# Kernel tuning notes

Measured on AMD Instinct MI355X. Metric: run time of the kernel, lower is better.

The kernel has to match this reference:

```python
import jax, jax.numpy as jnp
import numpy as np

N, E = 50000, 800000
D, DE = 128, 64
BN_EPS = 1e-5


def _bn(h, gamma, beta):
    # BatchNorm1d in training mode: biased batch statistics over the node axis
    mu = jnp.mean(h, axis=0)
    var = jnp.var(h, axis=0)
    return (h - mu) * jax.lax.rsqrt(var + BN_EPS) * gamma + beta


def setup_inputs() -> dict:
    key = jax.random.key(0)
    ks = jax.random.split(key, 12)
    s = lambda d: 1.0 / np.sqrt(d)
    return {
        "x": jax.random.normal(ks[0], (N, D), jnp.float32),
        "edge_index": jax.random.randint(ks[1], (2, E), 0, N, jnp.int64),
        "edge_attr_processed": jax.random.normal(ks[2], (E, DE), jnp.float32),
        # GINEConv edge linear: edge_dim -> node_dim
        "We": jax.random.uniform(ks[3], (D, DE), jnp.float32, -s(DE), s(DE)),
        "be": jnp.zeros((D,), jnp.float32),
        # MLP: Linear(D, 2D) -> BN(2D) -> ReLU -> Linear(2D, D)
        "W1": jax.random.uniform(ks[4], (2 * D, D), jnp.float32, -s(D), s(D)),
        "b1": jnp.zeros((2 * D,), jnp.float32),
        "g1": jnp.ones((2 * D,), jnp.float32),
        "beta1": jnp.zeros((2 * D,), jnp.float32),
        "W2": jax.random.uniform(ks[5], (D, 2 * D), jnp.float32, -s(2 * D), s(2 * D)),
        "b2": jnp.zeros((D,), jnp.float32),
        # outer BatchNorm(D)
        "g2": jnp.ones((D,), jnp.float32),
        "beta2": jnp.zeros((D,), jnp.float32),
        # GINE trainable eps (init 0.0)
        "eps": jnp.zeros((), jnp.float32),
    }


def reference(x, edge_index, edge_attr_processed, We, be, W1, b1, g1, beta1,
              W2, b2, g2, beta2, eps):
    src, dst = edge_index[0], edge_index[1]
    # GINEConv message: ReLU(x_j + Lin(edge_attr)); gather + edge add + relu
    msg = jax.nn.relu(x[src] + edge_attr_processed @ We.T + be)  # [E, D]
    # scatter-add aggregation at destination nodes
    agg = jax.ops.segment_sum(msg, dst, num_segments=x.shape[0])  # [N, D]
    h = (1.0 + eps) * x + agg
    # MLP: Linear -> BN -> ReLU -> Linear
    h = jax.nn.relu(_bn(h @ W1.T + b1, g1, beta1)) @ W2.T + b2
    # outer BN -> ReLU (dropout is identity at inference)
    return jax.nn.relu(_bn(h, g2, beta2))
```

## Files before the change

kernel.cpp:

```cpp
#include <hip/hip_runtime.h>
#include <stdint.h>
#include <stddef.h>


#define NN 50000
#define EE 800000
#define DD 128
#define DE 64
#define H1 256
#define NGRP 3125

typedef __attribute__((ext_vector_type(8))) short short8;
typedef __attribute__((ext_vector_type(4))) float floatx4;

__device__ __forceinline__ short f2bf(float f) {
    union { float f; uint32_t u; } v; v.f = f;
    return (short)((v.u + 0x7FFFu + ((v.u >> 16) & 1u)) >> 16);
}
__device__ __forceinline__ float bf2f(uint16_t u) {
    union { uint32_t u; float f; } v; v.u = (uint32_t)u << 16;
    return v.f;
}

__global__ __launch_bounds__(256) void swz_all_kernel(
    const float* __restrict__ We, const float* __restrict__ W1,
    const float* __restrict__ W2, short* __restrict__ dst) {
    int idx = blockIdx.x * 256 + threadIdx.x;
    if (idx >= 73728) return;
    const float* src; int KC, K, local; short* dp; bool efeat = false;
    if (idx < 8192)       { src = We; KC = 2; K = 64;  local = idx;          dp = dst; efeat = true; }
    else if (idx < 40960) { src = W1; KC = 4; K = 128; local = idx - 8192;  dp = dst + 8192; }
    else                  { src = W2; KC = 8; K = 256; local = idx - 40960; dp = dst + 40960; }
    int j = local & 7;
    int lane = (local >> 3) & 63;
    int f = local >> 9;
    int kc = f % KC;
    int nt = f / KC;
    int n = efeat ? ((lane & 15) * 8 + nt) : (nt * 16 + (lane & 15));
    int k = kc * 32 + ((lane >> 4) & 3) * 8 + j;
    dp[local] = f2bf(src[(size_t)n * K + k]);
}

__global__ __launch_bounds__(256) void count_kernel(const int* __restrict__ ei,
                                                    uint32_t* __restrict__ deg) {
    int e = blockIdx.x * 256 + threadIdx.x;
    atomicAdd(&deg[ei[EE + e]], 1u);
}

__global__ __launch_bounds__(256) void scan1_kernel(const uint32_t* __restrict__ deg,
                                                    uint32_t* __restrict__ partial) {
    __shared__ uint32_t ls[256];
    int i = blockIdx.x * 256 + threadIdx.x;
    ls[threadIdx.x] = deg[i];
    __syncthreads();
    for (int s = 128; s > 0; s >>= 1) {
        if (threadIdx.x < s) ls[threadIdx.x] += ls[threadIdx.x + s];
        __syncthreads();
    }
    if (threadIdx.x == 0) partial[blockIdx.x] = ls[0];
}

__global__ __launch_bounds__(256) void scan2_kernel(uint32_t* __restrict__ partial) {
    __shared__ uint32_t ls[196];
    if (threadIdx.x < 196) ls[threadIdx.x] = partial[threadIdx.x];
    __syncthreads();
    if (threadIdx.x == 0) {
        uint32_t run = 0;
        for (int i = 0; i < 196; ++i) { uint32_t t = ls[i]; ls[i] = run; run += t; }
    }
    __syncthreads();
    if (threadIdx.x < 196) partial[threadIdx.x] = ls[threadIdx.x];
}

__global__ __launch_bounds__(256) void scan3_kernel(const uint32_t* __restrict__ deg,
                                                    const uint32_t* __restrict__ partial,
                                                    uint32_t* __restrict__ base,
                                                    uint32_t* __restrict__ cursor) {
    __shared__ uint32_t ls[256];
    int i = blockIdx.x * 256 + threadIdx.x;
    uint32_t v = (i < NN) ? deg[i] : 0u;
    ls[threadIdx.x] = v;
    __syncthreads();
    for (int off = 1; off < 256; off <<= 1) {
        uint32_t t = (threadIdx.x >= off) ? ls[threadIdx.x - off] : 0u;
        __syncthreads();
        ls[threadIdx.x] += t;
        __syncthreads();
    }
    if (i < NN) {
        uint32_t b = partial[blockIdx.x] + ls[threadIdx.x] - v;
        base[i] = b;
        cursor[i] = b;
    } else if (i == NN) {
        base[NN] = EE;
    }
}

__global__ __launch_bounds__(256) void pos_kernel(const int* __restrict__ ei,
                                                  uint32_t* __restrict__ cursor,
                                                  uint32_t* __restrict__ pos) {
    int e = blockIdx.x * 256 + threadIdx.x;
    pos[e] = atomicAdd(&cursor[ei[EE + e]], 1u);
}

#define EDGE_GPW 5
__global__ __launch_bounds__(256) void edge_kernel(
    const float* __restrict__ x,
    const int* __restrict__ ei,
    const float* __restrict__ ea,
    const short* __restrict__ weswz,
    const float* __restrict__ be,
    const uint32_t* __restrict__ pos,
    uint16_t* __restrict__ msg)
{
    const int wave = threadIdx.x >> 6;
    const int lane = threadIdx.x & 63;
    const int l16 = lane & 15;
    const int q = lane >> 4;

    const short8* wp = (const short8*)weswz;
    short8 bfr[16];
#pragma unroll
    for (int f = 0; f < 16; ++f) bfr[f] = wp[f * 64 + lane];
    floatx4 bv0 = *(const floatx4*)(be + l16 * 8);
    floatx4 bv1 = *(const floatx4*)(be + l16 * 8 + 4);

    const int gbase = (blockIdx.x * 4 + wave) * EDGE_GPW;
    int sidx[4];
#pragma unroll
    for (int r = 0; r < 4; ++r) sidx[r] = ei[gbase * 16 + q * 4 + r];

#pragma unroll
    for (int g = 0; g < EDGE_GPW; ++g) {
        const int e0 = (gbase + g) * 16;
        floatx4 xa[4], xb[4];
#pragma unroll
        for (int r = 0; r < 4; ++r) {
            const float* xr = x + (size_t)sidx[r] * DD + l16 * 8;
            xa[r] = *(const floatx4*)(xr);
            xb[r] = *(const floatx4*)(xr + 4);
        }
        int sidxn[4];
        if (g + 1 < EDGE_GPW) {
#pragma unroll
            for (int r = 0; r < 4; ++r) sidxn[r] = ei[e0 + 16 + q * 4 + r];
        }
        uint32_t ppv[4];
#pragma unroll
        for (int r = 0; r < 4; ++r) ppv[r] = pos[e0 + q * 4 + r];

        const float* earow = ea + (size_t)(e0 + l16) * DE + q * 8;
        floatx4 p0 = *(const floatx4*)(earow);
        floatx4 p1 = *(const floatx4*)(earow + 4);
        floatx4 p2 = *(const floatx4*)(earow + 32);
        floatx4 p3 = *(const floatx4*)(earow + 36);
        short8 af0, af1;
#pragma unroll
        for (int j = 0; j < 4; ++j) {
            af0[j]     = f2bf(p0[j]);
            af0[j + 4] = f2bf(p1[j]);
            af1[j]     = f2bf(p2[j]);
            af1[j + 4] = f2bf(p3[j]);
        }
        floatx4 acc[8];
#pragma unroll
        for (int t = 0; t < 8; ++t) {
            floatx4 z = {0.f, 0.f, 0.f, 0.f};
            z = __builtin_amdgcn_mfma_f32_16x16x32_bf16(af0, bfr[t * 2], z, 0, 0, 0);
            acc[t] = __builtin_amdgcn_mfma_f32_16x16x32_bf16(af1, bfr[t * 2 + 1], z, 0, 0, 0);
        }
#pragma unroll
        for (int r = 0; r < 4; ++r) {
            uint32_t pk[4];
#pragma unroll
            for (int tt = 0; tt < 4; ++tt) {
                float X0 = (tt < 2) ? xa[r][2 * tt]     : xb[r][2 * tt - 4];
                float X1 = (tt < 2) ? xa[r][2 * tt + 1] : xb[r][2 * tt - 3];
                float B0 = (tt < 2) ? bv0[2 * tt]       : bv1[2 * tt - 4];
                float B1 = (tt < 2) ? bv0[2 * tt + 1]   : bv1[2 * tt - 3];
                float v0 = fmaxf(acc[2 * tt][r]     + B0 + X0, 0.f);
                float v1 = fmaxf(acc[2 * tt + 1][r] + B1 + X1, 0.f);
                pk[tt] = (uint32_t)(uint16_t)f2bf(v0) | ((uint32_t)(uint16_t)f2bf(v1) << 16);
            }
            uint4 val = {pk[0], pk[1], pk[2], pk[3]};
            *(uint4*)(msg + (size_t)ppv[r] * DD + l16 * 8) = val;
        }
        if (g + 1 < EDGE_GPW) {
#pragma unroll
            for (int r = 0; r < 4; ++r) sidx[r] = sidxn[r];
        }
    }
}

#define ACC8(u) do { \
    s0 += bf2f((uint16_t)((u).x & 0xFFFFu)); s1 += bf2f((uint16_t)((u).x >> 16)); \
    s2 += bf2f((uint16_t)((u).y & 0xFFFFu)); s3 += bf2f((uint16_t)((u).y >> 16)); \
    s4 += bf2f((uint16_t)((u).z & 0xFFFFu)); s5 += bf2f((uint16_t)((u).z >> 16)); \
    s6 += bf2f((uint16_t)((u).w & 0xFFFFu)); s7 += bf2f((uint16_t)((u).w >> 16)); } while (0)

__global__ __launch_bounds__(256) void reduce_kernel(
    const uint16_t* __restrict__ msg,
    const uint32_t* __restrict__ basep,
    const float* __restrict__ x,
    const float* __restrict__ epsp,
    uint16_t* __restrict__ hbf)
{
    const int n = blockIdx.x * 4 + (threadIdx.x >> 6);
    const int lane = threadIdx.x & 63;
    const int l16 = lane & 15;
    const int q = lane >> 4;
    const uint32_t b0 = basep[n];
    const uint32_t d = basep[n + 1] - b0;
    const uint4* bp = (const uint4*)((const uint32_t*)msg + (size_t)b0 * 64) + lane;
    float s0 = 0.f, s1 = 0.f, s2 = 0.f, s3 = 0.f;
    float s4 = 0.f, s5 = 0.f, s6 = 0.f, s7 = 0.f;
    const uint32_t nb = d >> 2;
    const uint32_t rem = d & 3u;
    uint32_t i = 0;
    for (; i + 2 <= nb; i += 2) {
        uint4 a = bp[(size_t)i * 64];
        uint4 b = bp[(size_t)(i + 1) * 64];
        ACC8(a); ACC8(b);
    }
    if (i < nb) { uint4 a = bp[(size_t)i * 64]; ACC8(a); }
    if ((uint32_t)q < rem) { uint4 a = bp[(size_t)nb * 64]; ACC8(a); }
    s0 += __shfl_xor(s0, 16); s0 += __shfl_xor(s0, 32);
    s1 += __shfl_xor(s1, 16); s1 += __shfl_xor(s1, 32);
    s2 += __shfl_xor(s2, 16); s2 += __shfl_xor(s2, 32);
    s3 += __shfl_xor(s3, 16); s3 += __shfl_xor(s3, 32);
    s4 += __shfl_xor(s4, 16); s4 += __shfl_xor(s4, 32);
    s5 += __shfl_xor(s5, 16); s5 += __shfl_xor(s5, 32);
    s6 += __shfl_xor(s6, 16); s6 += __shfl_xor(s6, 32);
    s7 += __shfl_xor(s7, 16); s7 += __shfl_xor(s7, 32);
    const float c1 = 1.0f + epsp[0];
    const float2 xv = *(const float2*)(x + (size_t)n * DD + (l16 * 4 + q) * 2);
    float a0 = (q == 0) ? s0 : (q == 1) ? s2 : (q == 2) ? s4 : s6;
    float a1 = (q == 0) ? s1 : (q == 1) ? s3 : (q == 2) ? s5 : s7;
    uint32_t pk = (uint32_t)(uint16_t)f2bf(c1 * xv.x + a0) |
                  ((uint32_t)(uint16_t)f2bf(c1 * xv.y + a1) << 16);
    ((uint32_t*)hbf)[(size_t)n * 64 + l16 * 4 + q] = pk;
}

__global__ __launch_bounds__(256) void gemm1_kernel(
    const uint16_t* __restrict__ hbf,
    const short* __restrict__ w1swz,
    const float* __restrict__ b1,
    uint16_t* __restrict__ t1,
    float* __restrict__ gsum,
    float* __restrict__ gsq)
{
    __shared__ float ls[H1];
    __shared__ float ls2[H1];
    const int tid = threadIdx.x;
    ls[tid] = 0.f; ls2[tid] = 0.f;
    __syncthreads();

    const int wave = tid >> 6;
    const int lane = tid & 63;
    const int l16 = lane & 15;
    const int q = lane >> 4;
    const short8* wp = (const short8*)w1swz;

    const int grp = blockIdx.x * 4 + wave;
    if (grp < NGRP) {
        const int n0 = grp * 16;
        const uint16_t* hr = hbf + (size_t)(n0 + l16) * DD + q * 8;
        short8 af[4];
#pragma unroll
        for (int kc = 0; kc < 4; ++kc) af[kc] = *(const short8*)(hr + kc * 32);
#pragma unroll
        for (int nt = 0; nt < 16; ++nt) {
            floatx4 acc = {0.f, 0.f, 0.f, 0.f};
#pragma unroll
            for (int kc = 0; kc < 4; ++kc)
                acc = __builtin_amdgcn_mfma_f32_16x16x32_bf16(
                    af[kc], wp[(nt * 4 + kc) * 64 + lane], acc, 0, 0, 0);
            const float bb = b1[nt * 16 + l16];
            float s = 0.f, s2 = 0.f;
#pragma unroll
            for (int r = 0; r < 4; ++r) {
                float v = acc[r] + bb;
                t1[(size_t)(n0 + q * 4 + r) * H1 + nt * 16 + l16] = (uint16_t)f2bf(v);
                s += v; s2 += v * v;
            }
            atomicAdd(&ls[nt * 16 + l16], s);
            atomicAdd(&ls2[nt * 16 + l16], s2);
        }
    }
    __syncthreads();
    atomicAdd(&gsum[tid], ls[tid]);
    atomicAdd(&gsq[tid], ls2[tid]);
}

__global__ __launch_bounds__(256) void gemm2_kernel(
    const uint16_t* __restrict__ t1,
    const float* __restrict__ scale1,
    const float* __restrict__ shift1,
    const short* __restrict__ w2swz,
    const float* __restrict__ b2,
    uint16_t* __restrict__ h2,
    float* __restrict__ gsum,
    float* __restrict__ gsq)
{
    __shared__ float ls[DD];
    __shared__ float ls2[DD];
    const int tid = threadIdx.x;
    if (tid < DD) { ls[tid] = 0.f; ls2[tid] = 0.f; }
    __syncthreads();

    const int wave = tid >> 6;
    const int lane = tid & 63;
    const int l16 = lane & 15;
    const int q = lane >> 4;
    const short8* wp = (const short8*)w2swz;

    const int grp = blockIdx.x * 4 + wave;
    if (grp < NGRP) {
        const int n0 = grp * 16;
        const uint16_t* tr = t1 + (size_t)(n0 + l16) * H1 + q * 8;
        floatx4 acc[8];
#pragma unroll
        for (int nt = 0; nt < 8; ++nt) acc[nt] = (floatx4){0.f, 0.f, 0.f, 0.f};
#pragma unroll
        for (int kc = 0; kc < 8; ++kc) {
            short8 tv = *(const short8*)(tr + kc * 32);
            const int kb = kc * 32 + q * 8;
            short8 af;
#pragma unroll
            for (int j = 0; j < 8; ++j) {
                float u = bf2f((uint16_t)tv[j]) * scale1[kb + j] + shift1[kb + j];
                af[j] = f2bf(fmaxf(u, 0.f));
            }
#pragma unroll
            for (int nt = 0; nt < 8; ++nt)
                acc[nt] = __builtin_amdgcn_mfma_f32_16x16x32_bf16(
                    af, wp[(nt * 8 + kc) * 64 + lane], acc[nt], 0, 0, 0);
        }
#pragma unroll
        for (int nt = 0; nt < 8; ++nt) {
            const float bb = b2[nt * 16 + l16];
            float s = 0.f, s2 = 0.f;
#pragma unroll
            for (int r = 0; r < 4; ++r) {
                float v = acc[nt][r] + bb;
                h2[(size_t)(n0 + q * 4 + r) * DD + nt * 16 + l16] = (uint16_t)f2bf(v);
                s += v; s2 += v * v;
            }
            atomicAdd(&ls[nt * 16 + l16], s);
            atomicAdd(&ls2[nt * 16 + l16], s2);
        }
    }
    __syncthreads();
    if (tid < DD) {
        atomicAdd(&gsum[tid], ls[tid]);
        atomicAdd(&gsq[tid], ls2[tid]);
    }
}

__global__ void finalize_kernel(const float* __restrict__ ssum,
                                const float* __restrict__ ssumsq,
                                const float* __restrict__ gamma,
                                const float* __restrict__ beta,
                                float* __restrict__ scale,
                                float* __restrict__ shift, int C) {
    int c = threadIdx.x;
    if (c >= C) return;
    float mu = ssum[c] * (1.0f / NN);
    float var = ssumsq[c] * (1.0f / NN) - mu * mu;
    float rs = rsqrtf(var + 1e-5f);
    float sc = gamma[c] * rs;
    scale[c] = sc;
    shift[c] = beta[c] - mu * sc;
}

__global__ __launch_bounds__(256) void out_kernel(const uint16_t* __restrict__ h2,
                                                  const float* __restrict__ scale2,
                                                  const float* __restrict__ shift2,
                                                  float* __restrict__ out) {
    int idx = blockIdx.x * 256 + threadIdx.x;
    int base = idx * 8;
    int c = base & (DD - 1);
    uint4 pk = *(const uint4*)(h2 + base);
    const uint32_t u[4] = {pk.x, pk.y, pk.z, pk.w};
    floatx4 o0, o1;
#pragma unroll
    for (int j = 0; j < 4; ++j) {
        float vlo = bf2f((uint16_t)(u[j] & 0xFFFFu));
        float vhi = bf2f((uint16_t)(u[j] >> 16));
        int cc = c + j * 2;
        float a = fmaxf(vlo * scale2[cc] + shift2[cc], 0.f);
        float b = fmaxf(vhi * scale2[cc + 1] + shift2[cc + 1], 0.f);
        if (j < 2) { o0[j * 2] = a; o0[j * 2 + 1] = b; }
        else       { o1[(j - 2) * 2] = a; o1[(j - 2) * 2 + 1] = b; }
    }
    *(floatx4*)(out + base) = o0;
    *(floatx4*)(out + base + 4) = o1;
}

extern "C" void kernel_launch(void* const* d_in, const int* in_sizes, int n_in,
                              void* d_out, int out_size, void* d_ws, size_t ws_size,
                              hipStream_t stream) {
    const float* x     = (const float*)d_in[0];
    const int*   ei    = (const int*)d_in[1];
    const float* ea    = (const float*)d_in[2];
    const float* We    = (const float*)d_in[3];
    const float* be    = (const float*)d_in[4];
    const float* W1    = (const float*)d_in[5];
    const float* b1    = (const float*)d_in[6];
    const float* g1    = (const float*)d_in[7];
    const float* beta1 = (const float*)d_in[8];
    const float* W2    = (const float*)d_in[9];
    const float* b2    = (const float*)d_in[10];
    const float* g2    = (const float*)d_in[11];
    const float* beta2 = (const float*)d_in[12];
    const float* epsp  = (const float*)d_in[13];

    float* ws      = (float*)d_ws;
    float* gsum1   = ws + 0;
    float* gsq1    = ws + 256;
    float* gsum2   = ws + 512;
    float* gsq2    = ws + 640;
    float* scale1  = ws + 768;
    float* shift1  = ws + 1024;
    float* scale2  = ws + 1280;
    float* shift2  = ws + 1408;
    uint32_t* deg     = (uint32_t*)(ws + 1536);
    uint32_t* basep   = deg + 50176;
    uint32_t* cursor  = basep + 50432;
    uint32_t* partial = cursor + 50176;
    uint32_t* pos     = partial + 256;
    uint16_t* hbf     = (uint16_t*)(pos + EE);
    uint16_t* msg     = hbf + (size_t)NN * DD;
    uint16_t* t1      = msg;
    uint16_t* h2      = t1 + (size_t)NN * H1;
    short*    wswz    = (short*)(msg + (size_t)EE * DD);
    short*    weswz   = wswz;
    short*    w1swz   = wswz + 8192;
    short*    w2swz   = wswz + 40960;

    hipMemsetAsync(ws, 0, (1536 + 50176) * sizeof(uint32_t), stream);

    swz_all_kernel<<<dim3(288), 256, 0, stream>>>(We, W1, W2, wswz);
    count_kernel<<<dim3(3125), 256, 0, stream>>>(ei, deg);
    scan1_kernel<<<dim3(196), 256, 0, stream>>>(deg, partial);
    scan2_kernel<<<dim3(1), 256, 0, stream>>>(partial);
    scan3_kernel<<<dim3(196), 256, 0, stream>>>(deg, partial, basep, cursor);
    pos_kernel<<<dim3(3125), 256, 0, stream>>>(ei, cursor, pos);

    edge_kernel<<<dim3(2500), 256, 0, stream>>>(x, ei, ea, weswz, be, pos, msg);
    reduce_kernel<<<dim3(12500), 256, 0, stream>>>(msg, basep, x, epsp, hbf);

    gemm1_kernel<<<dim3(782), 256, 0, stream>>>(hbf, w1swz, b1, t1, gsum1, gsq1);
    finalize_kernel<<<dim3(1), 256, 0, stream>>>(gsum1, gsq1, g1, beta1, scale1, shift1, H1);

    gemm2_kernel<<<dim3(782), 256, 0, stream>>>(t1, scale1, shift1, w2swz, b2, h2, gsum2, gsq2);
    finalize_kernel<<<dim3(1), 128, 0, stream>>>(gsum2, gsq2, g2, beta2, scale2, shift2, DD);

    out_kernel<<<dim3(3125), 256, 0, stream>>>(h2, scale2, shift2, (float*)d_out);
}
```

Before: 611.5 us.

## Fuse CSR slot claiming into edge kernel and vectorize GEMM epilogue stores

Removes the separate pos kernel and its 3.2 MB pos array: the edge kernel now claims each edge's destination slot with an atomicAdd on the cursor and broadcasts it to the lanes with shuffles. Separately, the W1/W2 swizzle permutes output columns so each lane owns contiguous output columns. This lets the gemm1/gemm2 epilogues pack bf16 pairs into 16-byte stores and reduce BN statistics across quads with shuffles before the shared-memory atomics. The atomics inside the edge kernel may add latency on its critical path, and the per-edge slot order within a segment becomes nondeterministic.

```diff
diff --git a/kernel.cpp b/kernel.cpp
--- a/kernel.cpp
+++ b/kernel.cpp
@@ -27,16 +27,16 @@
     const float* __restrict__ W2, short* __restrict__ dst) {
     int idx = blockIdx.x * 256 + threadIdx.x;
     if (idx >= 73728) return;
-    const float* src; int KC, K, local; short* dp; bool efeat = false;
-    if (idx < 8192)       { src = We; KC = 2; K = 64;  local = idx;          dp = dst; efeat = true; }
-    else if (idx < 40960) { src = W1; KC = 4; K = 128; local = idx - 8192;  dp = dst + 8192; }
-    else                  { src = W2; KC = 8; K = 256; local = idx - 40960; dp = dst + 40960; }
+    const float* src; int KC, K, NT, local; short* dp;
+    if (idx < 8192)       { src = We; KC = 2; K = 64;  NT = 8;  local = idx;          dp = dst; }
+    else if (idx < 40960) { src = W1; KC = 4; K = 128; NT = 16; local = idx - 8192;  dp = dst + 8192; }
+    else                  { src = W2; KC = 8; K = 256; NT = 8;  local = idx - 40960; dp = dst + 40960; }
     int j = local & 7;
     int lane = (local >> 3) & 63;
     int f = local >> 9;
     int kc = f % KC;
     int nt = f / KC;
-    int n = efeat ? ((lane & 15) * 8 + nt) : (nt * 16 + (lane & 15));
+    int n = (lane & 15) * NT + nt;
     int k = kc * 32 + ((lane >> 4) & 3) * 8 + j;
     dp[local] = f2bf(src[(size_t)n * K + k]);
 }
@@ -96,13 +96,6 @@
     }
 }
 
-__global__ __launch_bounds__(256) void pos_kernel(const int* __restrict__ ei,
-                                                  uint32_t* __restrict__ cursor,
-                                                  uint32_t* __restrict__ pos) {
-    int e = blockIdx.x * 256 + threadIdx.x;
-    pos[e] = atomicAdd(&cursor[ei[EE + e]], 1u);
-}
-
 #define EDGE_GPW 5
 __global__ __launch_bounds__(256) void edge_kernel(
     const float* __restrict__ x,
@@ -110,7 +103,7 @@
     const float* __restrict__ ea,
     const short* __restrict__ weswz,
     const float* __restrict__ be,
-    const uint32_t* __restrict__ pos,
+    uint32_t* __restrict__ cursor,
     uint16_t* __restrict__ msg)
 {
     const int wave = threadIdx.x >> 6;
@@ -133,6 +126,14 @@
 #pragma unroll
     for (int g = 0; g < EDGE_GPW; ++g) {
         const int e0 = (gbase + g) * 16;
+        uint32_t claim = 0u;
+        if (lane < 16) {
+            int dv = ei[EE + e0 + lane];
+            claim = atomicAdd(&cursor[dv], 1u);
+        }
+        uint32_t ppv[4];
+#pragma unroll
+        for (int r = 0; r < 4; ++r) ppv[r] = __shfl(claim, q * 4 + r);
         floatx4 xa[4], xb[4];
 #pragma unroll
         for (int r = 0; r < 4; ++r) {
@@ -145,10 +146,6 @@
 #pragma unroll
             for (int r = 0; r < 4; ++r) sidxn[r] = ei[e0 + 16 + q * 4 + r];
         }
-        uint32_t ppv[4];
-#pragma unroll
-        for (int r = 0; r < 4; ++r) ppv[r] = pos[e0 + q * 4 + r];
-
         const float* earow = ea + (size_t)(e0 + l16) * DE + q * 8;
         floatx4 p0 = *(const floatx4*)(earow);
         floatx4 p1 = *(const floatx4*)(earow + 4);
@@ -269,22 +266,50 @@
 #pragma unroll
         for (int kc = 0; kc < 4; ++kc) af[kc] = *(const short8*)(hr + kc * 32);
 #pragma unroll
-        for (int nt = 0; nt < 16; ++nt) {
-            floatx4 acc = {0.f, 0.f, 0.f, 0.f};
-#pragma unroll
-            for (int kc = 0; kc < 4; ++kc)
-                acc = __builtin_amdgcn_mfma_f32_16x16x32_bf16(
-                    af[kc], wp[(nt * 4 + kc) * 64 + lane], acc, 0, 0, 0);
-            const float bb = b1[nt * 16 + l16];
-            float s = 0.f, s2 = 0.f;
+        for (int pass = 0; pass < 2; ++pass) {
+            floatx4 a8[8];
+#pragma unroll
+            for (int t = 0; t < 8; ++t) a8[t] = (floatx4){0.f, 0.f, 0.f, 0.f};
+#pragma unroll
+            for (int t = 0; t < 8; ++t) {
+                const int nt = pass * 8 + t;
+#pragma unroll
+                for (int kc = 0; kc < 4; ++kc)
+                    a8[t] = __builtin_amdgcn_mfma_f32_16x16x32_bf16(
+                        af[kc], wp[(nt * 4 + kc) * 64 + lane], a8[t], 0, 0, 0);
+            }
+            floatx4 bva = *(const floatx4*)(b1 + l16 * 16 + pass * 8);
+            floatx4 bvb = *(const floatx4*)(b1 + l16 * 16 + pass * 8 + 4);
+            float sa[8], s2a[8];
+#pragma unroll
+            for (int t = 0; t < 8; ++t) { sa[t] = 0.f; s2a[t] = 0.f; }
 #pragma unroll
             for (int r = 0; r < 4; ++r) {
-                float v = acc[r] + bb;
-                t1[(size_t)(n0 + q * 4 + r) * H1 + nt * 16 + l16] = (uint16_t)f2bf(v);
-                s += v; s2 += v * v;
-            }
-            atomicAdd(&ls[nt * 16 + l16], s);
-            atomicAdd(&ls2[nt * 16 + l16], s2);
+                uint32_t pk[4];
+#pragma unroll
+                for (int t2 = 0; t2 < 4; ++t2) {
+                    float B0 = (t2 < 2) ? bva[2 * t2]     : bvb[2 * t2 - 4];
+                    float B1 = (t2 < 2) ? bva[2 * t2 + 1] : bvb[2 * t2 - 3];
+                    float v0 = a8[2 * t2][r] + B0;
+                    float v1 = a8[2 * t2 + 1][r] + B1;
+                    sa[2 * t2] += v0; s2a[2 * t2] += v0 * v0;
+                    sa[2 * t2 + 1] += v1; s2a[2 * t2 + 1] += v1 * v1;
+                    pk[t2] = (uint32_t)(uint16_t)f2bf(v0) |
+                             ((uint32_t)(uint16_t)f2bf(v1) << 16);
+                }
+                *(uint4*)(t1 + (size_t)(n0 + q * 4 + r) * H1 + l16 * 16 + pass * 8) =
+                    (uint4){pk[0], pk[1], pk[2], pk[3]};
+            }
+#pragma unroll
+            for (int t = 0; t < 8; ++t) {
+                float s = sa[t], s2 = s2a[t];
+                s += __shfl_xor(s, 16);  s += __shfl_xor(s, 32);
+                s2 += __shfl_xor(s2, 16); s2 += __shfl_xor(s2, 32);
+                if (q == 0) {
+                    atomicAdd(&ls[l16 * 16 + pass * 8 + t], s);
+                    atomicAdd(&ls2[l16 * 16 + pass * 8 + t], s2);
+                }
+            }
         }
     }
     __syncthreads();
@@ -336,18 +361,37 @@
                 acc[nt] = __builtin_amdgcn_mfma_f32_16x16x32_bf16(
                     af, wp[(nt * 8 + kc) * 64 + lane], acc[nt], 0, 0, 0);
         }
-#pragma unroll
-        for (int nt = 0; nt < 8; ++nt) {
-            const float bb = b2[nt * 16 + l16];
-            float s = 0.f, s2 = 0.f;
-#pragma unroll
-            for (int r = 0; r < 4; ++r) {
-                float v = acc[nt][r] + bb;
-                h2[(size_t)(n0 + q * 4 + r) * DD + nt * 16 + l16] = (uint16_t)f2bf(v);
-                s += v; s2 += v * v;
-            }
-            atomicAdd(&ls[nt * 16 + l16], s);
-            atomicAdd(&ls2[nt * 16 + l16], s2);
+        floatx4 bva = *(const floatx4*)(b2 + l16 * 8);
+        floatx4 bvb = *(const floatx4*)(b2 + l16 * 8 + 4);
+        float sa[8], s2a[8];
+#pragma unroll
+        for (int t = 0; t < 8; ++t) { sa[t] = 0.f; s2a[t] = 0.f; }
+#pragma unroll
+        for (int r = 0; r < 4; ++r) {
+            uint32_t pk[4];
+#pragma unroll
+            for (int t2 = 0; t2 < 4; ++t2) {
+                float B0 = (t2 < 2) ? bva[2 * t2]     : bvb[2 * t2 - 4];
+                float B1 = (t2 < 2) ? bva[2 * t2 + 1] : bvb[2 * t2 - 3];
+                float v0 = acc[2 * t2][r] + B0;
+                float v1 = acc[2 * t2 + 1][r] + B1;
+                sa[2 * t2] += v0; s2a[2 * t2] += v0 * v0;
+                sa[2 * t2 + 1] += v1; s2a[2 * t2 + 1] += v1 * v1;
+                pk[t2] = (uint32_t)(uint16_t)f2bf(v0) |
+                         ((uint32_t)(uint16_t)f2bf(v1) << 16);
+            }
+            *(uint4*)(h2 + (size_t)(n0 + q * 4 + r) * DD + l16 * 8) =
+                (uint4){pk[0], pk[1], pk[2], pk[3]};
+        }
+#pragma unroll
+        for (int t = 0; t < 8; ++t) {
+            float s = sa[t], s2 = s2a[t];
+            s += __shfl_xor(s, 16);  s += __shfl_xor(s, 32);
+            s2 += __shfl_xor(s2, 16); s2 += __shfl_xor(s2, 32);
+            if (q == 0) {
+                atomicAdd(&ls[l16 * 8 + t], s);
+                atomicAdd(&ls2[l16 * 8 + t], s2);
+            }
         }
     }
     __syncthreads();
@@ -428,8 +472,7 @@
     uint32_t* basep   = deg + 50176;
     uint32_t* cursor  = basep + 50432;
     uint32_t* partial = cursor + 50176;
-    uint32_t* pos     = partial + 256;
-    uint16_t* hbf     = (uint16_t*)(pos + EE);
+    uint16_t* hbf     = (uint16_t*)(partial + 256);
     uint16_t* msg     = hbf + (size_t)NN * DD;
     uint16_t* t1      = msg;
     uint16_t* h2      = t1 + (size_t)NN * H1;
@@ -445,9 +488,8 @@
     scan1_kernel<<<dim3(196), 256, 0, stream>>>(deg, partial);
     scan2_kernel<<<dim3(1), 256, 0, stream>>>(partial);
     scan3_kernel<<<dim3(196), 256, 0, stream>>>(deg, partial, basep, cursor);
-    pos_kernel<<<dim3(3125), 256, 0, stream>>>(ei, cursor, pos);
-
-    edge_kernel<<<dim3(2500), 256, 0, stream>>>(x, ei, ea, weswz, be, pos, msg);
+
+    edge_kernel<<<dim3(2500), 256, 0, stream>>>(x, ei, ea, weswz, be, cursor, msg);
     reduce_kernel<<<dim3(12500), 256, 0, stream>>>(msg, basep, x, epsp, hbf);
 
     gemm1_kernel<<<dim3(782), 256, 0, stream>>>(hbf, w1swz, b1, t1, gsum1, gsq1);
```

Measured after the change: 572.5 us. 1.07x faster.
